# Kernel optimization log

Hardware: AMD Instinct MI355X
Metric: run time of the kernel (lower is better)

Reference implementation:

```python
import jax, jax.numpy as jnp
import numpy as np

E = 512        # embedding_dim
HEADS = 8
PD = 32        # patch_dim
STRIDE = 16    # unfold stride (hard-coded in source)
P = 16         # max regions per image (padded)
NCLS = 3       # num_classes
LN_EPS = 1e-5


def layer_norm(x, g, b):
    mu = x.mean(-1, keepdims=True)
    v = ((x - mu) ** 2).mean(-1, keepdims=True)
    return (x - mu) / jnp.sqrt(v + LN_EPS) * g + b


def patch2vec(x, Wr, br):
    # x: [N, C, PD, PD]; AdaptiveAvgPool3d to (C//4, PD//2, PD//2) with exact
    # integer ratios == block-mean pooling, then Linear(fvector, E).
    N, C, H, W = x.shape
    y = x.reshape(N, C // 4, 4, H // 2, 2, W // 2, 2).mean(axis=(2, 4, 6))
    return y.reshape(N, -1) @ Wr.T + br


def mha(q_in, kv_in, Wqkv, bqkv, Wo, bo):
    # torch nn.MultiheadAttention, batch_first=True
    B, Pq, _ = q_in.shape
    L = kv_in.shape[1]
    hd = E // HEADS
    Wq, Wk, Wv = Wqkv[:E], Wqkv[E:2 * E], Wqkv[2 * E:]
    bq, bk, bv = bqkv[:E], bqkv[E:2 * E], bqkv[2 * E:]
    q = (q_in @ Wq.T + bq).reshape(B, Pq, HEADS, hd)
    k = (kv_in @ Wk.T + bk).reshape(B, L, HEADS, hd)
    v = (kv_in @ Wv.T + bv).reshape(B, L, HEADS, hd)
    scores = jnp.einsum('bphd,blhd->bhpl', q, k) / jnp.sqrt(jnp.asarray(hd, q.dtype))
    attn = jax.nn.softmax(scores, axis=-1)
    out = jnp.einsum('bhpl,blhd->bphd', attn, v).reshape(B, Pq, E)
    return out @ Wo.T + bo


def setup_inputs() -> dict:
    key = jax.random.key(0)
    ks = jax.random.split(key, 12)
    B, C, H, W = 8, 64, 256, 256
    fv = (C // 4) * (PD // 2) * (PD // 2)  # 4096
    s = lambda n: 1.0 / np.sqrt(n)
    return {
        'features': jax.random.normal(ks[0], (B, C, H, W), jnp.float32),
        'probs': jax.random.uniform(ks[1], (B, NCLS, H, W), jnp.float32),
        'patches': jax.random.normal(ks[2], (B, P, C, PD, PD), jnp.float32),
        'masks': jax.random.randint(ks[3], (B, H, W), 0, P + 1, jnp.int32),
        'ln_g': jnp.ones((E,), jnp.float32),
        'ln_b': jnp.zeros((E,), jnp.float32),
        'Wr': jax.random.normal(ks[4], (E, fv), jnp.float32) * s(fv),
        'br': jnp.zeros((E,), jnp.float32),
        'Wqkv': jax.random.normal(ks[5], (3 * E, E), jnp.float32) * s(E),
        'bqkv': jnp.zeros((3 * E,), jnp.float32),
        'Wo': jax.random.normal(ks[6], (E, E), jnp.float32) * s(E),
        'bo': jnp.zeros((E,), jnp.float32),
        'Wm': jax.random.normal(ks[7], (E, E), jnp.float32) * s(E),
        'bm': jnp.zeros((E,), jnp.float32),
        'Wc': jax.random.normal(ks[8], (NCLS - 1, E), jnp.float32) * s(E),
        'bc': jnp.zeros((NCLS - 1,), jnp.float32),
    }


def reference(features, probs, patches, masks, ln_g, ln_b, Wr, br,
              Wqkv, bqkv, Wo, bo, Wm, bm, Wc, bc):
    B, C, H, W = features.shape
    # ---- unfold features into overlapping PDxPD blocks, stride 16 ----
    n = (H - PD) // STRIDE + 1  # 15
    rows = (jnp.arange(n) * STRIDE)[:, None] + jnp.arange(PD)[None, :]  # [n, PD]
    xb = features[:, :, rows, :]          # [B, C, n, PD, W]
    blocks = xb[:, :, :, :, rows]         # [B, C, n, PD, n, PD]
    blocks = blocks.transpose(0, 2, 4, 1, 3, 5).reshape(B, n * n, C, PD, PD)
    L = n * n

    # ---- shared Patch2vec embedding + shared LayerNorm ----
    pe = layer_norm(patch2vec(patches.reshape(B * P, C, PD, PD), Wr, br).reshape(B, P, E), ln_g, ln_b)
    be = layer_norm(patch2vec(blocks.reshape(B * L, C, PD, PD), Wr, br).reshape(B, L, E), ln_g, ln_b)

    # ---- attention + residual MLP ----
    attn = mha(pe, be, Wqkv, bqkv, Wo, bo)
    res = layer_norm(attn + pe, ln_g, ln_b)
    x = jax.nn.gelu(res @ Wm.T + bm, approximate=False) + res
    outs = x @ Wc.T + bc  # [B, P, 2]

    # ---- vectorized masked reclassify (regions are disjoint) ----
    labels = masks  # [B, H, W], 0 = background, 1..P = regions
    seg = (labels.astype(jnp.int32) + jnp.arange(B, dtype=jnp.int32)[:, None, None] * (P + 1)).reshape(-1)
    pr = probs.transpose(0, 2, 3, 1).reshape(-1, NCLS)
    sums = jax.ops.segment_sum(pr, seg, num_segments=B * (P + 1)).reshape(B, P + 1, NCLS)
    cnt = jax.ops.segment_sum(jnp.ones((pr.shape[0],), pr.dtype), seg, num_segments=B * (P + 1)).reshape(B, P + 1)
    mean = sums / jnp.maximum(cnt, 1.0)[..., None] + 1e-6  # orig_mean_logits per region
    ml = mean[:, 1:, :]  # [B, P, NCLS], region labels 1..P <-> logits 0..P-1
    new0 = ml[..., 0] / (0.5 * (ml[..., 1] + ml[..., 2])) * outs.mean(-1)
    newv = jnp.stack([new0, outs[..., 0], outs[..., 1]], axis=-1)  # [B, P, 3]
    newv_full = jnp.concatenate([jnp.zeros((B, 1, NCLS), newv.dtype), newv], axis=1)
    vals = newv_full[jnp.arange(B)[:, None], labels.reshape(B, -1)]  # [B, H*W, 3]
    vals = vals.reshape(B, H, W, NCLS).transpose(0, 3, 1, 2)
    return jnp.where((labels > 0)[:, None, :, :], vals, probs)
```

## Files before the change

### kernel.cpp

```cpp
#include <hip/hip_runtime.h>
#include <stdint.h>


typedef __attribute__((ext_vector_type(8))) short bf16x8;
typedef __attribute__((ext_vector_type(4))) float f32x4;

__device__ __forceinline__ unsigned short f2bf(float x) {
    union { float f; unsigned u; } v; v.f = x;
    unsigned r = v.u + 0x7FFFu + ((v.u >> 16) & 1u);
    return (unsigned short)(r >> 16);
}
__device__ __forceinline__ float bf2f(unsigned short x) {
    union { unsigned u; float f; } v; v.u = ((unsigned)x) << 16; return v.f;
}

__device__ __forceinline__ void g2l16(const unsigned short* g, unsigned short* l) {
    __builtin_amdgcn_global_load_lds(
        (const __attribute__((address_space(1))) unsigned int*)g,
        (__attribute__((address_space(3))) unsigned int*)l, 16, 0, 0);
}

__global__ __launch_bounds__(256) void k_prep(
    const float* __restrict__ f, const float* __restrict__ p,
    const float* __restrict__ Wr, const float* __restrict__ Wqkv,
    const float* __restrict__ Wo, const float* __restrict__ Wm,
    unsigned short* __restrict__ gp, unsigned short* __restrict__ Xb,
    unsigned short* __restrict__ oWr, unsigned short* __restrict__ oWqkv,
    unsigned short* __restrict__ oWo, unsigned short* __restrict__ oWm,
    float* __restrict__ seg)
{
    int blk = blockIdx.x, tid = threadIdx.x;
    if (blk < 8192) {
        if (blk == 0) for (int i = tid; i < 544; i += 256) seg[i] = 0.f;
        unsigned t = blk * 256u + tid;
        unsigned q = t & 127u, r = (t >> 7) & 127u, g = (t >> 14) & 15u, b = t >> 18;
        const float2* f2 = (const float2*)f;
        float s = 0.f;
        unsigned cb = b * 64u + g * 4u;
#pragma unroll
        for (int j = 0; j < 4; ++j)
#pragma unroll
            for (int a = 0; a < 2; ++a) {
                unsigned idx = ((cb + j) * 256u + 2u * r + a) * 256u + 2u * q;
                float2 v = f2[idx >> 1];
                s += v.x + v.y;
            }
        gp[t] = f2bf(s * 0.0625f);
    } else if (blk < 10240) {
        unsigned t = (blk - 8192) * 256u + tid;
        unsigned i = t & 4095u, row = t >> 12;
        unsigned q = i & 15u, r = (i >> 4) & 15u, g = i >> 8;
        const float2* p2 = (const float2*)p;
        float s = 0.f;
        unsigned cb = row * 64u + g * 4u;
#pragma unroll
        for (int j = 0; j < 4; ++j)
#pragma unroll
            for (int a = 0; a < 2; ++a) {
                unsigned idx = ((cb + j) * 32u + 2u * r + a) * 32u + 2u * q;
                float2 v = p2[idx >> 1];
                s += v.x + v.y;
            }
        Xb[(size_t)row * 4096 + i] = f2bf(s * 0.0625f);
    } else {
        int t = (blk - 10240) * 256 + tid;
        const float* src; unsigned short* dst; int i;
        if (t < 524288)      { src = Wr;   dst = oWr;   i = t; }
        else if (t < 720896) { src = Wqkv; dst = oWqkv; i = t - 524288; }
        else if (t < 786432) { src = Wo;   dst = oWo;   i = t - 720896; }
        else                 { src = Wm;   dst = oWm;   i = t - 786432; }
        float4 v = ((const float4*)src)[i];
        ushort4 o;
        o.x = f2bf(v.x); o.y = f2bf(v.y); o.z = f2bf(v.z); o.w = f2bf(v.w);
        ((ushort4*)dst)[i] = o;
    }
}

template<bool GATHER>
__global__ __launch_bounds__(256) void k_gemm128(
    const unsigned short* __restrict__ A, const unsigned short* __restrict__ Gp,
    const unsigned short* __restrict__ Bw,
    const float* __restrict__ bias, float* __restrict__ C,
    int M, int N, int K, int klen)
{
    __shared__ __align__(16) unsigned short As[128 * 32];
    __shared__ __align__(16) unsigned short Bs[128 * 32];
    const int tid = threadIdx.x, w = tid >> 6, lane = tid & 63;
    const int nt = blockIdx.x, mt = blockIdx.y, ks = blockIdx.z;
    const int kbase = ks * klen;
    const int l15 = lane & 15, kq = (lane >> 4) * 8;
    const int wm = (w >> 1) * 64, wn = (w & 1) * 64;
    const int srow0 = w * 32, lrow = lane >> 2, lcol = (lane & 3) * 8;

    size_t arowbase[2]; bool apatch[2];
#pragma unroll
    for (int c = 0; c < 2; ++c) {
        int r = srow0 + c * 16 + lrow;
        int ga = mt * 128 + r; if (ga > M - 1) ga = M - 1;
        if (GATHER && ga >= 128) {
            int rr = ga - 128;
            int bb = rr / 225, ij = rr - bb * 225;
            int ii = ij / 15, jj = ij - ii * 15;
            arowbase[c] = (size_t)bb * 262144 + ii * 1024 + jj * 8;
            apatch[c] = false;
        } else {
            arowbase[c] = (size_t)ga * K;
            apatch[c] = true;
        }
    }
    const int brow0 = nt * 128;

    f32x4 acc[4][4];
#pragma unroll
    for (int i = 0; i < 4; ++i)
#pragma unroll
        for (int j = 0; j < 4; ++j) acc[i][j] = (f32x4){0.f, 0.f, 0.f, 0.f};

    for (int k0 = 0; k0 < klen; k0 += 32) {
        int kk = kbase + k0;
        int kcol = kk + lcol;
#pragma unroll
        for (int c = 0; c < 2; ++c) {
            const unsigned short* gp_a;
            if (!GATHER || apatch[c]) {
                gp_a = A + arowbase[c] + kcol;
            } else {
                gp_a = Gp + arowbase[c] + ((size_t)(kcol >> 8) << 14)
                     + (((kcol >> 4) & 15) << 7) + (kcol & 15);
            }
            g2l16(gp_a, &As[(srow0 + c * 16) * 32]);
            g2l16(Bw + (size_t)(brow0 + srow0 + c * 16 + lrow) * K + kcol,
                  &Bs[(srow0 + c * 16) * 32]);
        }
        __syncthreads();
        bf16x8 af[4], bf[4];
#pragma unroll
        for (int i = 0; i < 4; ++i) {
            af[i] = *(const bf16x8*)&As[(wm + 16 * i + l15) * 32 + kq];
            bf[i] = *(const bf16x8*)&Bs[(wn + 16 * i + l15) * 32 + kq];
        }
#pragma unroll
        for (int i = 0; i < 4; ++i)
#pragma unroll
            for (int j = 0; j < 4; ++j)
                acc[i][j] = __builtin_amdgcn_mfma_f32_16x16x32_bf16(af[i], bf[j], acc[i][j], 0, 0, 0);
        __syncthreads();
    }
    float* Cp = C + (size_t)ks * M * N;
#pragma unroll
    for (int i = 0; i < 4; ++i) {
        int rowb = mt * 128 + wm + i * 16 + (lane >> 4) * 4;
#pragma unroll
        for (int j = 0; j < 4; ++j) {
            int col = nt * 128 + wn + j * 16 + l15;
            float bv = bias ? bias[col] : 0.f;
#pragma unroll
            for (int r = 0; r < 4; ++r) {
                int row = rowb + r;
                if (row < M) Cp[(size_t)row * N + col] = acc[i][j][r] + bv;
            }
        }
    }
}

__global__ __launch_bounds__(256) void k_lnred(
    const float* __restrict__ Yp, const float* __restrict__ br,
    const float* __restrict__ gg, const float* __restrict__ bb,
    float* __restrict__ outF, unsigned short* __restrict__ outB,
    int rows, int nsplit)
{
    int wave = threadIdx.x >> 6, lane = threadIdx.x & 63;
    int row = blockIdx.x * 4 + wave;
    if (row >= rows) return;
    size_t base = (size_t)row * 512 + lane * 8;
    float v[8];
    { const float* bp = br + lane * 8;
      float4 a = *(const float4*)bp, b = *(const float4*)(bp + 4);
      v[0]=a.x; v[1]=a.y; v[2]=a.z; v[3]=a.w; v[4]=b.x; v[5]=b.y; v[6]=b.z; v[7]=b.w; }
    for (int s = 0; s < nsplit; ++s) {
        const float* xp = Yp + (size_t)s * rows * 512 + base;
        float4 a = *(const float4*)xp, b = *(const float4*)(xp + 4);
        v[0]+=a.x; v[1]+=a.y; v[2]+=a.z; v[3]+=a.w; v[4]+=b.x; v[5]+=b.y; v[6]+=b.z; v[7]+=b.w;
    }
    float s = 0.f;
#pragma unroll
    for (int i = 0; i < 8; ++i) s += v[i];
#pragma unroll
    for (int m = 32; m; m >>= 1) s += __shfl_xor(s, m, 64);
    float mu = s * (1.f / 512.f);
    float sq = 0.f;
#pragma unroll
    for (int i = 0; i < 8; ++i) { float d = v[i] - mu; sq += d * d; }
#pragma unroll
    for (int m = 32; m; m >>= 1) sq += __shfl_xor(sq, m, 64);
    float rstd = rsqrtf(sq * (1.f / 512.f) + 1e-5f);
    const float* gp = gg + lane * 8;
    const float* bp2 = bb + lane * 8;
    float4 g0 = *(const float4*)gp, g1 = *(const float4*)(gp + 4);
    float4 b0 = *(const float4*)bp2, b1 = *(const float4*)(bp2 + 4);
    float ga[8] = {g0.x,g0.y,g0.z,g0.w,g1.x,g1.y,g1.z,g1.w};
    float ba[8] = {b0.x,b0.y,b0.z,b0.w,b1.x,b1.y,b1.z,b1.w};
    float o[8];
#pragma unroll
    for (int i = 0; i < 8; ++i) o[i] = (v[i] - mu) * rstd * ga[i] + ba[i];
    float* ofp = outF + base;
    float4 w0; w0.x=o[0]; w0.y=o[1]; w0.z=o[2]; w0.w=o[3];
    float4 w1; w1.x=o[4]; w1.y=o[5]; w1.z=o[6]; w1.w=o[7];
    *(float4*)ofp = w0; *(float4*)(ofp + 4) = w1;
    unsigned short* obp = outB + base;
    ushort4 u0, u1;
    u0.x=f2bf(o[0]); u0.y=f2bf(o[1]); u0.z=f2bf(o[2]); u0.w=f2bf(o[3]);
    u1.x=f2bf(o[4]); u1.y=f2bf(o[5]); u1.z=f2bf(o[6]); u1.w=f2bf(o[7]);
    ((ushort4*)obp)[0] = u0; ((ushort4*)obp)[1] = u1;
}

__global__ __launch_bounds__(256) void k_attn(
    const float* __restrict__ QKV, unsigned short* __restrict__ attn_bf)
{
    const int b = blockIdx.x, h = blockIdx.y, pz = blockIdx.z;
    __shared__ __align__(16) float qs[4 * 64];
    __shared__ __align__(16) unsigned short Ks[225 * 68];
    __shared__ __align__(16) unsigned short Vs[225 * 64];
    __shared__ float sc[4 * 225];
    const int t = threadIdx.x;

    {
        int p = t >> 6, d = t & 63;
        qs[t] = QKV[(size_t)(b * 16 + pz * 4 + p) * 1536 + h * 64 + d];
    }
    for (int i = t; i < 14400; i += 256) {
        int l = i >> 6, d = i & 63;
        size_t base = (size_t)(128 + b * 225 + l) * 1536 + h * 64 + d;
        Ks[l * 68 + d] = f2bf(QKV[base + 512]);
        Vs[l * 64 + d] = f2bf(QKV[base + 1024]);
    }
    __syncthreads();
    for (int i = t; i < 900; i += 256) {
        int p = i / 225, l = i - p * 225;
        const ushort4* k4 = (const ushort4*)&Ks[l * 68];
        const float4* q4 = (const float4*)&qs[p * 64];
        float s = 0.f;
#pragma unroll
        for (int d = 0; d < 16; ++d) {
            ushort4 kk = k4[d]; float4 qq = q4[d];
            s += bf2f(kk.x) * qq.x + bf2f(kk.y) * qq.y
               + bf2f(kk.z) * qq.z + bf2f(kk.w) * qq.w;
        }
        sc[p * 225 + l] = s * 0.125f;
    }
    __syncthreads();
    const int lane = t & 63, wave = t >> 6;
    {
        float* row = &sc[wave * 225];
        float m = -1e30f;
        for (int l = lane; l < 225; l += 64) m = fmaxf(m, row[l]);
#pragma unroll
        for (int off = 32; off; off >>= 1) m = fmaxf(m, __shfl_xor(m, off, 64));
        float s = 0.f;
        for (int l = lane; l < 225; l += 64) { float e = __expf(row[l] - m); row[l] = e; s += e; }
#pragma unroll
        for (int off = 32; off; off >>= 1) s += __shfl_xor(s, off, 64);
        float inv = 1.f / s;
        for (int l = lane; l < 225; l += 64) row[l] *= inv;
    }
    __syncthreads();
    {
        float o = 0.f;
        const float* scp = &sc[wave * 225];
        for (int l = 0; l < 225; ++l) o += scp[l] * bf2f(Vs[l * 64 + lane]);
        attn_bf[(size_t)(b * 16 + pz * 4 + wave) * 512 + h * 64 + lane] = f2bf(o);
    }
}

__global__ __launch_bounds__(256) void k_tail(
    const unsigned short* __restrict__ attnb, const unsigned short* __restrict__ Wo_b,
    const float* __restrict__ bo, const float* __restrict__ LNf,
    const float* __restrict__ gg, const float* __restrict__ bb,
    const unsigned short* __restrict__ Wm_b, const float* __restrict__ bm,
    const float* __restrict__ Wc, const float* __restrict__ bc,
    float* __restrict__ outs)
{
    __shared__ __align__(16) unsigned short Abuf[16 * 520];
    __shared__ __align__(16) unsigned short Bs[4][128 * 32];
    __shared__ float Zf[16 * 512];
    __shared__ float part[16][4][2];
    const int tid = threadIdx.x, w = tid >> 6, lane = tid & 63;
    const int l15 = lane & 15, quad = lane >> 4, kq = quad * 8;
    const int r0 = blockIdx.x * 16;

#pragma unroll
    for (int c = 0; c < 4; ++c) {
        int row = c * 4 + w;
        g2l16(attnb + (size_t)(r0 + row) * 512 + lane * 8, &Abuf[row * 520]);
    }

    f32x4 acc[8];
#pragma unroll
    for (int i = 0; i < 8; ++i) acc[i] = (f32x4){0.f, 0.f, 0.f, 0.f};

    for (int k0 = 0; k0 < 512; k0 += 32) {
#pragma unroll
        for (int c = 0; c < 8; ++c) {
            int n = w * 128 + c * 16 + (lane >> 2);
            g2l16(Wo_b + (size_t)n * 512 + k0 + (lane & 3) * 8, &Bs[w][(c * 16) * 32]);
        }
        __syncthreads();
        bf16x8 af = *(const bf16x8*)&Abuf[l15 * 520 + k0 + kq];
#pragma unroll
        for (int i = 0; i < 8; ++i) {
            bf16x8 bf = *(const bf16x8*)&Bs[w][(i * 16 + l15) * 32 + kq];
            acc[i] = __builtin_amdgcn_mfma_f32_16x16x32_bf16(af, bf, acc[i], 0, 0, 0);
        }
        __syncthreads();
    }
#pragma unroll
    for (int i = 0; i < 8; ++i) {
        int col = w * 128 + i * 16 + l15;
        float bv = bo[col];
#pragma unroll
        for (int r = 0; r < 4; ++r)
            Zf[(quad * 4 + r) * 512 + col] = acc[i][r] + bv;
    }
    __syncthreads();

    for (int pass = 0; pass < 4; ++pass) {
        int row = pass * 4 + w;
        float v[8];
#pragma unroll
        for (int i = 0; i < 8; ++i)
            v[i] = Zf[row * 512 + lane * 8 + i] + LNf[(size_t)(r0 + row) * 512 + lane * 8 + i];
        float s = 0.f;
#pragma unroll
        for (int i = 0; i < 8; ++i) s += v[i];
#pragma unroll
        for (int m = 32; m; m >>= 1) s += __shfl_xor(s, m, 64);
        float mu = s * (1.f / 512.f);
        float sq = 0.f;
#pragma unroll
        for (int i = 0; i < 8; ++i) { float d = v[i] - mu; sq += d * d; }
#pragma unroll
        for (int m = 32; m; m >>= 1) sq += __shfl_xor(sq, m, 64);
        float rstd = rsqrtf(sq * (1.f / 512.f) + 1e-5f);
#pragma unroll
        for (int i = 0; i < 8; ++i) {
            int col = lane * 8 + i;
            float o = (v[i] - mu) * rstd * gg[col] + bb[col];
            Zf[row * 512 + col] = o;
            Abuf[row * 520 + col] = f2bf(o);
        }
    }
    __syncthreads();

#pragma unroll
    for (int i = 0; i < 8; ++i) acc[i] = (f32x4){0.f, 0.f, 0.f, 0.f};
    for (int k0 = 0; k0 < 512; k0 += 32) {
#pragma unroll
        for (int c = 0; c < 8; ++c) {
            int n = w * 128 + c * 16 + (lane >> 2);
            g2l16(Wm_b + (size_t)n * 512 + k0 + (lane & 3) * 8, &Bs[w][(c * 16) * 32]);
        }
        __syncthreads();
        bf16x8 af = *(const bf16x8*)&Abuf[l15 * 520 + k0 + kq];
#pragma unroll
        for (int i = 0; i < 8; ++i) {
            bf16x8 bf = *(const bf16x8*)&Bs[w][(i * 16 + l15) * 32 + kq];
            acc[i] = __builtin_amdgcn_mfma_f32_16x16x32_bf16(af, bf, acc[i], 0, 0, 0);
        }
        __syncthreads();
    }
    float s0[4] = {0,0,0,0}, s1[4] = {0,0,0,0};
#pragma unroll
    for (int i = 0; i < 8; ++i) {
        int col = w * 128 + i * 16 + l15;
        float wc0 = Wc[col], wc1 = Wc[512 + col], bmv = bm[col];
#pragma unroll
        for (int r = 0; r < 4; ++r) {
            float v = acc[i][r] + bmv;
            float x = 0.5f * v * (1.f + erff(v * 0.70710678118654752f))
                    + Zf[(quad * 4 + r) * 512 + col];
            s0[r] += x * wc0; s1[r] += x * wc1;
        }
    }
#pragma unroll
    for (int off = 8; off; off >>= 1)
#pragma unroll
        for (int r = 0; r < 4; ++r) {
            s0[r] += __shfl_xor(s0[r], off, 16);
            s1[r] += __shfl_xor(s1[r], off, 16);
        }
    if (l15 == 0)
#pragma unroll
        for (int r = 0; r < 4; ++r) {
            part[quad * 4 + r][w][0] = s0[r];
            part[quad * 4 + r][w][1] = s1[r];
        }
    __syncthreads();
    if (tid < 32) {
        int row = tid >> 1, c = tid & 1;
        float s = part[row][0][c] + part[row][1][c] + part[row][2][c] + part[row][3][c];
        outs[(r0 + row) * 2 + c] = s + bc[c];
    }
}

__global__ __launch_bounds__(256) void k_hist(
    const int* __restrict__ masks, const float* __restrict__ probs,
    float* __restrict__ sums, float* __restrict__ cnt)
{
    __shared__ float ls[4][68];
    int t = threadIdx.x, wave = t >> 6;
    for (int i = t; i < 272; i += 256) ((float*)ls)[i] = 0.f;
    __syncthreads();
    int b = blockIdx.x >> 6, chunk = blockIdx.x & 63;
    int base = chunk * 1024;
    for (int it = 0; it < 4; ++it) {
        int px = base + it * 256 + t;
        int lab = masks[b * 65536 + px];
        atomicAdd(&ls[wave][lab * 3 + 0], probs[(size_t)(b * 3 + 0) * 65536 + px]);
        atomicAdd(&ls[wave][lab * 3 + 1], probs[(size_t)(b * 3 + 1) * 65536 + px]);
        atomicAdd(&ls[wave][lab * 3 + 2], probs[(size_t)(b * 3 + 2) * 65536 + px]);
        atomicAdd(&ls[wave][51 + lab], 1.f);
    }
    __syncthreads();
    if (t < 68) {
        float v = ls[0][t] + ls[1][t] + ls[2][t] + ls[3][t];
        if (t < 51) atomicAdd(&sums[b * 51 + t], v);
        else        atomicAdd(&cnt[b * 17 + t - 51], v);
    }
}

__global__ __launch_bounds__(256) void k_out(
    const int* __restrict__ masks, const float* __restrict__ probs,
    const float* __restrict__ seg, const float* __restrict__ outs,
    float* __restrict__ out)
{
    __shared__ float nv[17 * 3];
    int tid = threadIdx.x;
    int b = blockIdx.x >> 8;
    if (tid < 17) {
        int lab = tid;
        if (lab == 0) { nv[0] = 0.f; nv[1] = 0.f; nv[2] = 0.f; }
        else {
            float c  = fmaxf(seg[408 + b * 17 + lab], 1.f);
            float m0 = seg[(b * 17 + lab) * 3 + 0] / c + 1e-6f;
            float m1 = seg[(b * 17 + lab) * 3 + 1] / c + 1e-6f;
            float m2 = seg[(b * 17 + lab) * 3 + 2] / c + 1e-6f;
            int p = lab - 1;
            float o0 = outs[(b * 16 + p) * 2 + 0], o1 = outs[(b * 16 + p) * 2 + 1];
            nv[lab * 3 + 0] = m0 / (0.5f * (m1 + m2)) * (0.5f * (o0 + o1));
            nv[lab * 3 + 1] = o0;
            nv[lab * 3 + 2] = o1;
        }
    }
    __syncthreads();
    int px = (blockIdx.x & 255) * 256 + tid;
    int gl = b * 65536 + px;
    int lab = masks[gl];
    if (lab > 0) {
        out[(size_t)(b*3+0)*65536 + px] = nv[lab*3+0];
        out[(size_t)(b*3+1)*65536 + px] = nv[lab*3+1];
        out[(size_t)(b*3+2)*65536 + px] = nv[lab*3+2];
    } else {
        out[(size_t)(b*3+0)*65536 + px] = probs[(size_t)(b*3+0)*65536 + px];
        out[(size_t)(b*3+1)*65536 + px] = probs[(size_t)(b*3+1)*65536 + px];
        out[(size_t)(b*3+2)*65536 + px] = probs[(size_t)(b*3+2)*65536 + px];
    }
}

extern "C" void kernel_launch(void* const* d_in, const int* in_sizes, int n_in,
                              void* d_out, int out_size, void* d_ws, size_t ws_size,
                              hipStream_t stream)
{
    const float* features = (const float*)d_in[0];
    const float* probs    = (const float*)d_in[1];
    const float* patches  = (const float*)d_in[2];
    const int*   masks    = (const int*)d_in[3];
    const float* ln_g     = (const float*)d_in[4];
    const float* ln_b     = (const float*)d_in[5];
    const float* Wr       = (const float*)d_in[6];
    const float* br       = (const float*)d_in[7];
    const float* Wqkv     = (const float*)d_in[8];
    const float* bqkv     = (const float*)d_in[9];
    const float* Wo       = (const float*)d_in[10];
    const float* bo       = (const float*)d_in[11];
    const float* Wm       = (const float*)d_in[12];
    const float* bm       = (const float*)d_in[13];
    const float* Wc       = (const float*)d_in[14];
    const float* bc       = (const float*)d_in[15];
    float* out = (float*)d_out;

    char* w = (char*)d_ws;
    size_t off = 0;
    auto alloc = [&](size_t bytes) -> char* {
        char* p = w + off;
        off += (bytes + 255) & ~(size_t)255;
        return p;
    };
    unsigned short* Gp     = (unsigned short*)alloc((size_t)2097152 * 2);
    unsigned short* Xb     = (unsigned short*)alloc((size_t)128 * 4096 * 2);
    unsigned short* Wr_b   = (unsigned short*)alloc((size_t)2097152 * 2);
    unsigned short* Wqkv_b = (unsigned short*)alloc((size_t)786432 * 2);
    unsigned short* Wo_b   = (unsigned short*)alloc((size_t)262144 * 2);
    unsigned short* Wm_b   = (unsigned short*)alloc((size_t)262144 * 2);
    float* Yp   = (float*)alloc((size_t)8 * 1928 * 512 * 4);
    float* LNf  = (float*)alloc((size_t)1928 * 512 * 4);
    unsigned short* LNb = (unsigned short*)alloc((size_t)1928 * 512 * 2);
    float* QKV  = (float*)alloc((size_t)1928 * 1536 * 4);
    unsigned short* attnb = (unsigned short*)alloc((size_t)65536 * 2);
    float* outsB = (float*)alloc((size_t)256 * 4);
    float* seg   = (float*)alloc((size_t)544 * 4);

    k_prep<<<13568, 256, 0, stream>>>(features, patches, Wr, Wqkv, Wo, Wm,
                                      Gp, Xb, Wr_b, Wqkv_b, Wo_b, Wm_b, seg);
    k_hist<<<512, 256, 0, stream>>>(masks, probs, seg, seg + 408);
    k_gemm128<true><<<dim3(4, 16, 8), 256, 0, stream>>>(
        Xb, Gp, Wr_b, nullptr, Yp, 1928, 512, 4096, 512);
    k_lnred<<<482, 256, 0, stream>>>(Yp, br, ln_g, ln_b, LNf, LNb, 1928, 8);
    k_gemm128<false><<<dim3(12, 16, 1), 256, 0, stream>>>(
        LNb, nullptr, Wqkv_b, bqkv, QKV, 1928, 1536, 512, 512);
    k_attn<<<dim3(8, 8, 4), 256, 0, stream>>>(QKV, attnb);
    k_tail<<<8, 256, 0, stream>>>(attnb, Wo_b, bo, LNf, ln_g, ln_b,
                                  Wm_b, bm, Wc, bc, outsB);
    k_out<<<2048, 256, 0, stream>>>(masks, probs, seg, outsB, out);
}
```

Measured before the change: 370.6 us.

## Vectorize pooling loads, emit bf16 QKV, trim LN writes, widen tail K-step

The feature pooling in k_prep now reads float4 and produces two pooled outputs per thread, which halves that block count. The QKV GEMM writes bf16 output directly, and k_attn loads K/V with 16-byte vector loads instead of converting fp32 per element. The LayerNorm kernel writes fp32 output only for the first 128 rows, the only rows used later. The tail kernel's two small GEMMs step K by 64 instead of 32, halving barriers at the cost of a larger LDS buffer. Q is now rounded to bf16, which lowers precision slightly.

```diff
diff --git a/kernel.cpp b/kernel.cpp
--- a/kernel.cpp
+++ b/kernel.cpp
@@ -30,24 +30,24 @@
     float* __restrict__ seg)
 {
     int blk = blockIdx.x, tid = threadIdx.x;
-    if (blk < 8192) {
+    if (blk < 4096) {
         if (blk == 0) for (int i = tid; i < 544; i += 256) seg[i] = 0.f;
         unsigned t = blk * 256u + tid;
-        unsigned q = t & 127u, r = (t >> 7) & 127u, g = (t >> 14) & 15u, b = t >> 18;
-        const float2* f2 = (const float2*)f;
-        float s = 0.f;
+        unsigned q2 = t & 63u, r = (t >> 6) & 127u, g = (t >> 13) & 15u, b = t >> 17;
+        const float4* f4 = (const float4*)f;
+        float s0 = 0.f, s1 = 0.f;
         unsigned cb = b * 64u + g * 4u;
 #pragma unroll
         for (int j = 0; j < 4; ++j)
 #pragma unroll
             for (int a = 0; a < 2; ++a) {
-                unsigned idx = ((cb + j) * 256u + 2u * r + a) * 256u + 2u * q;
-                float2 v = f2[idx >> 1];
-                s += v.x + v.y;
+                float4 v = f4[((cb + j) * 256u + 2u * r + a) * 64u + q2];
+                s0 += v.x + v.y; s1 += v.z + v.w;
             }
-        gp[t] = f2bf(s * 0.0625f);
-    } else if (blk < 10240) {
-        unsigned t = (blk - 8192) * 256u + tid;
+        ushort2 o; o.x = f2bf(s0 * 0.0625f); o.y = f2bf(s1 * 0.0625f);
+        ((ushort2*)gp)[((b * 16u + g) * 128u + r) * 64u + q2] = o;
+    } else if (blk < 6144) {
+        unsigned t = (blk - 4096) * 256u + tid;
         unsigned i = t & 4095u, row = t >> 12;
         unsigned q = i & 15u, r = (i >> 4) & 15u, g = i >> 8;
         const float2* p2 = (const float2*)p;
@@ -63,7 +63,7 @@
             }
         Xb[(size_t)row * 4096 + i] = f2bf(s * 0.0625f);
     } else {
-        int t = (blk - 10240) * 256 + tid;
+        int t = (blk - 6144) * 256 + tid;
         const float* src; unsigned short* dst; int i;
         if (t < 524288)      { src = Wr;   dst = oWr;   i = t; }
         else if (t < 720896) { src = Wqkv; dst = oWqkv; i = t - 524288; }
@@ -76,11 +76,12 @@
     }
 }
 
-template<bool GATHER>
+template<bool GATHER, bool BF16OUT>
 __global__ __launch_bounds__(256) void k_gemm128(
     const unsigned short* __restrict__ A, const unsigned short* __restrict__ Gp,
     const unsigned short* __restrict__ Bw,
     const float* __restrict__ bias, float* __restrict__ C,
+    unsigned short* __restrict__ Cb,
     int M, int N, int K, int klen)
 {
     __shared__ __align__(16) unsigned short As[128 * 32];
@@ -117,8 +118,7 @@
         for (int j = 0; j < 4; ++j) acc[i][j] = (f32x4){0.f, 0.f, 0.f, 0.f};
 
     for (int k0 = 0; k0 < klen; k0 += 32) {
-        int kk = kbase + k0;
-        int kcol = kk + lcol;
+        int kcol = kbase + k0 + lcol;
 #pragma unroll
         for (int c = 0; c < 2; ++c) {
             const unsigned short* gp_a;
@@ -157,7 +157,10 @@
 #pragma unroll
             for (int r = 0; r < 4; ++r) {
                 int row = rowb + r;
-                if (row < M) Cp[(size_t)row * N + col] = acc[i][j][r] + bv;
+                if (row < M) {
+                    if (BF16OUT) Cb[(size_t)row * N + col] = f2bf(acc[i][j][r] + bv);
+                    else         Cp[(size_t)row * N + col] = acc[i][j][r] + bv;
+                }
             }
         }
     }
@@ -203,10 +206,12 @@
     float o[8];
 #pragma unroll
     for (int i = 0; i < 8; ++i) o[i] = (v[i] - mu) * rstd * ga[i] + ba[i];
-    float* ofp = outF + base;
-    float4 w0; w0.x=o[0]; w0.y=o[1]; w0.z=o[2]; w0.w=o[3];
-    float4 w1; w1.x=o[4]; w1.y=o[5]; w1.z=o[6]; w1.w=o[7];
-    *(float4*)ofp = w0; *(float4*)(ofp + 4) = w1;
+    if (row < 128) {
+        float* ofp = outF + base;
+        float4 w0; w0.x=o[0]; w0.y=o[1]; w0.z=o[2]; w0.w=o[3];
+        float4 w1; w1.x=o[4]; w1.y=o[5]; w1.z=o[6]; w1.w=o[7];
+        *(float4*)ofp = w0; *(float4*)(ofp + 4) = w1;
+    }
     unsigned short* obp = outB + base;
     ushort4 u0, u1;
     u0.x=f2bf(o[0]); u0.y=f2bf(o[1]); u0.z=f2bf(o[2]); u0.w=f2bf(o[3]);
@@ -215,7 +220,7 @@
 }
 
 __global__ __launch_bounds__(256) void k_attn(
-    const float* __restrict__ QKV, unsigned short* __restrict__ attn_bf)
+    const unsigned short* __restrict__ QKVb, unsigned short* __restrict__ attn_bf)
 {
     const int b = blockIdx.x, h = blockIdx.y, pz = blockIdx.z;
     __shared__ __align__(16) float qs[4 * 64];
@@ -226,13 +231,15 @@
 
     {
         int p = t >> 6, d = t & 63;
-        qs[t] = QKV[(size_t)(b * 16 + pz * 4 + p) * 1536 + h * 64 + d];
-    }
-    for (int i = t; i < 14400; i += 256) {
-        int l = i >> 6, d = i & 63;
-        size_t base = (size_t)(128 + b * 225 + l) * 1536 + h * 64 + d;
-        Ks[l * 68 + d] = f2bf(QKV[base + 512]);
-        Vs[l * 64 + d] = f2bf(QKV[base + 1024]);
+        qs[t] = bf2f(QKVb[(size_t)(b * 16 + pz * 4 + p) * 1536 + h * 64 + d]);
+    }
+    for (int i = t; i < 1800; i += 256) {
+        int l = i >> 3, d8 = (i & 7) * 8;
+        size_t base = (size_t)(128 + b * 225 + l) * 1536 + h * 64 + d8;
+        uint4 kk4 = *(const uint4*)(QKVb + base + 512);
+        *(uint2*)&Ks[l * 68 + d8]     = make_uint2(kk4.x, kk4.y);
+        *(uint2*)&Ks[l * 68 + d8 + 4] = make_uint2(kk4.z, kk4.w);
+        *(uint4*)&Vs[l * 64 + d8] = *(const uint4*)(QKVb + base + 1024);
     }
     __syncthreads();
     for (int i = t; i < 900; i += 256) {
@@ -281,7 +288,7 @@
     float* __restrict__ outs)
 {
     __shared__ __align__(16) unsigned short Abuf[16 * 520];
-    __shared__ __align__(16) unsigned short Bs[4][128 * 32];
+    __shared__ __align__(16) unsigned short Bs[4][128 * 64];
     __shared__ float Zf[16 * 512];
     __shared__ float part[16][4][2];
     const int tid = threadIdx.x, w = tid >> 6, lane = tid & 63;
@@ -298,18 +305,21 @@
 #pragma unroll
     for (int i = 0; i < 8; ++i) acc[i] = (f32x4){0.f, 0.f, 0.f, 0.f};
 
-    for (int k0 = 0; k0 < 512; k0 += 32) {
-#pragma unroll
-        for (int c = 0; c < 8; ++c) {
-            int n = w * 128 + c * 16 + (lane >> 2);
-            g2l16(Wo_b + (size_t)n * 512 + k0 + (lane & 3) * 8, &Bs[w][(c * 16) * 32]);
+    for (int k0 = 0; k0 < 512; k0 += 64) {
+#pragma unroll
+        for (int c = 0; c < 16; ++c) {
+            int n = w * 128 + c * 8 + (lane >> 3);
+            g2l16(Wo_b + (size_t)n * 512 + k0 + (lane & 7) * 8, &Bs[w][c * 512]);
         }
         __syncthreads();
-        bf16x8 af = *(const bf16x8*)&Abuf[l15 * 520 + k0 + kq];
+        bf16x8 af0 = *(const bf16x8*)&Abuf[l15 * 520 + k0 + kq];
+        bf16x8 af1 = *(const bf16x8*)&Abuf[l15 * 520 + k0 + 32 + kq];
 #pragma unroll
         for (int i = 0; i < 8; ++i) {
-            bf16x8 bf = *(const bf16x8*)&Bs[w][(i * 16 + l15) * 32 + kq];
-            acc[i] = __builtin_amdgcn_mfma_f32_16x16x32_bf16(af, bf, acc[i], 0, 0, 0);
+            bf16x8 b0 = *(const bf16x8*)&Bs[w][(i * 16 + l15) * 64 + kq];
+            bf16x8 b1 = *(const bf16x8*)&Bs[w][(i * 16 + l15) * 64 + 32 + kq];
+            acc[i] = __builtin_amdgcn_mfma_f32_16x16x32_bf16(af0, b0, acc[i], 0, 0, 0);
+            acc[i] = __builtin_amdgcn_mfma_f32_16x16x32_bf16(af1, b1, acc[i], 0, 0, 0);
         }
         __syncthreads();
     }
@@ -353,18 +363,21 @@
 
 #pragma unroll
     for (int i = 0; i < 8; ++i) acc[i] = (f32x4){0.f, 0.f, 0.f, 0.f};
-    for (int k0 = 0; k0 < 512; k0 += 32) {
-#pragma unroll
-        for (int c = 0; c < 8; ++c) {
-            int n = w * 128 + c * 16 + (lane >> 2);
-            g2l16(Wm_b + (size_t)n * 512 + k0 + (lane & 3) * 8, &Bs[w][(c * 16) * 32]);
+    for (int k0 = 0; k0 < 512; k0 += 64) {
+#pragma unroll
+        for (int c = 0; c < 16; ++c) {
+            int n = w * 128 + c * 8 + (lane >> 3);
+            g2l16(Wm_b + (size_t)n * 512 + k0 + (lane & 7) * 8, &Bs[w][c * 512]);
         }
         __syncthreads();
-        bf16x8 af = *(const bf16x8*)&Abuf[l15 * 520 + k0 + kq];
+        bf16x8 af0 = *(const bf16x8*)&Abuf[l15 * 520 + k0 + kq];
+        bf16x8 af1 = *(const bf16x8*)&Abuf[l15 * 520 + k0 + 32 + kq];
 #pragma unroll
         for (int i = 0; i < 8; ++i) {
-            bf16x8 bf = *(const bf16x8*)&Bs[w][(i * 16 + l15) * 32 + kq];
-            acc[i] = __builtin_amdgcn_mfma_f32_16x16x32_bf16(af, bf, acc[i], 0, 0, 0);
+            bf16x8 b0 = *(const bf16x8*)&Bs[w][(i * 16 + l15) * 64 + kq];
+            bf16x8 b1 = *(const bf16x8*)&Bs[w][(i * 16 + l15) * 64 + 32 + kq];
+            acc[i] = __builtin_amdgcn_mfma_f32_16x16x32_bf16(af0, b0, acc[i], 0, 0, 0);
+            acc[i] = __builtin_amdgcn_mfma_f32_16x16x32_bf16(af1, b1, acc[i], 0, 0, 0);
         }
         __syncthreads();
     }
@@ -502,22 +515,22 @@
     unsigned short* Wo_b   = (unsigned short*)alloc((size_t)262144 * 2);
     unsigned short* Wm_b   = (unsigned short*)alloc((size_t)262144 * 2);
     float* Yp   = (float*)alloc((size_t)8 * 1928 * 512 * 4);
-    float* LNf  = (float*)alloc((size_t)1928 * 512 * 4);
-    unsigned short* LNb = (unsigned short*)alloc((size_t)1928 * 512 * 2);
-    float* QKV  = (float*)alloc((size_t)1928 * 1536 * 4);
+    float* LNf  = (float*)alloc((size_t)128 * 512 * 4);
+    unsigned short* LNb  = (unsigned short*)alloc((size_t)1928 * 512 * 2);
+    unsigned short* QKVb = (unsigned short*)alloc((size_t)1928 * 1536 * 2);
     unsigned short* attnb = (unsigned short*)alloc((size_t)65536 * 2);
     float* outsB = (float*)alloc((size_t)256 * 4);
     float* seg   = (float*)alloc((size_t)544 * 4);
 
-    k_prep<<<13568, 256, 0, stream>>>(features, patches, Wr, Wqkv, Wo, Wm,
-                                      Gp, Xb, Wr_b, Wqkv_b, Wo_b, Wm_b, seg);
+    k_prep<<<9472, 256, 0, stream>>>(features, patches, Wr, Wqkv, Wo, Wm,
+                                     Gp, Xb, Wr_b, Wqkv_b, Wo_b, Wm_b, seg);
     k_hist<<<512, 256, 0, stream>>>(masks, probs, seg, seg + 408);
-    k_gemm128<true><<<dim3(4, 16, 8), 256, 0, stream>>>(
-        Xb, Gp, Wr_b, nullptr, Yp, 1928, 512, 4096, 512);
+    k_gemm128<true, false><<<dim3(4, 16, 8), 256, 0, stream>>>(
+        Xb, Gp, Wr_b, nullptr, Yp, nullptr, 1928, 512, 4096, 512);
     k_lnred<<<482, 256, 0, stream>>>(Yp, br, ln_g, ln_b, LNf, LNb, 1928, 8);
-    k_gemm128<false><<<dim3(12, 16, 1), 256, 0, stream>>>(
-        LNb, nullptr, Wqkv_b, bqkv, QKV, 1928, 1536, 512, 512);
-    k_attn<<<dim3(8, 8, 4), 256, 0, stream>>>(QKV, attnb);
+    k_gemm128<false, true><<<dim3(12, 16, 1), 256, 0, stream>>>(
+        LNb, nullptr, Wqkv_b, bqkv, nullptr, QKVb, 1928, 1536, 512, 512);
+    k_attn<<<dim3(8, 8, 4), 256, 0, stream>>>(QKVb, attnb);
     k_tail<<<8, 256, 0, stream>>>(attnb, Wo_b, bo, LNf, ln_g, ln_b,
                                   Wm_b, bm, Wc, bc, outsB);
     k_out<<<2048, 256, 0, stream>>>(masks, probs, seg, outsB, out);
```

Result: faster. 363.0 us (-2.0%).
